# Kernel tuning notes

Hardware: AMD Instinct MI355X
Metric: run time of the kernel (lower is better)

Reference implementation:

```python
import jax, jax.numpy as jnp
import numpy as np

NUM_OBJS = 180   # len(vocab['node'])
NUM_PREDS = 180  # len(vocab['edge'])
D = 128          # embedding_dim == gconv_dim
H = 512          # gconv_hidden_dim
L = 5            # gconv_num_layers (1 GraphTripleConv + 4 in GraphTripleConvNet; identical shapes)
G = 64           # number of graphs in the batch
O = 5000         # total nodes
T = 20000        # total triples (edges)
SC = 0.02        # param init scale


def setup_inputs() -> dict:
    key = jax.random.key(0)
    ks = jax.random.split(key, 18)
    objs = jax.random.randint(ks[0], (O,), 0, NUM_OBJS + 1)
    s = jax.random.randint(ks[1], (T,), 0, O)
    o = jax.random.randint(ks[2], (T,), 0, O)
    p = jax.random.randint(ks[3], (T,), 0, NUM_PREDS)
    triples = jnp.stack([s, p, o], axis=1)
    obj_to_img = jnp.sort(jax.random.randint(ks[4], (O,), 0, G))
    f32 = jnp.float32
    return {
        'objs': objs,
        'triples': triples,
        'obj_to_img': obj_to_img,
        'obj_emb': jax.random.normal(ks[5], (NUM_OBJS + 1, D), f32) * SC,
        'pred_emb': jax.random.normal(ks[6], (NUM_PREDS, D), f32) * SC,
        # net1: [3D -> H -> 2H + D], stacked over L layers
        'n1w1': jax.random.normal(ks[7], (L, 3 * D, H), f32) * SC,
        'n1b1': jnp.zeros((L, H), f32),
        'n1w2': jax.random.normal(ks[8], (L, H, 2 * H + D), f32) * SC,
        'n1b2': jnp.zeros((L, 2 * H + D), f32),
        # net2: [H -> H -> D], stacked over L layers
        'n2w1': jax.random.normal(ks[9], (L, H, H), f32) * SC,
        'n2b1': jnp.zeros((L, H), f32),
        'n2w2': jax.random.normal(ks[10], (L, H, D), f32) * SC,
        'n2b2': jnp.zeros((L, D), f32),
        # AttentionModule: per-graph attention pooling over node vectors
        'att_w': jax.random.normal(ks[11], (D,), f32) * SC,
        'att_b': jnp.zeros((), f32),
    }


def _mlp2(x, w1, b1, w2, b2):
    # build_mlp with final_nonlinearity=True -> Linear,ReLU,Linear,ReLU
    return jax.nn.relu(jax.nn.relu(x @ w1 + b1) @ w2 + b2)


def _triple_conv(ov, pv, s, o, n1w1, n1b1, n1w2, n1b2, n2w1, n2b1, n2w2, n2b2):
    n_obj = ov.shape[0]
    t = jnp.concatenate([ov[s], pv, ov[o]], axis=1)          # [T, 3D]
    new_t = _mlp2(t, n1w1, n1b1, n1w2, n1b2)                 # [T, 2H+D]
    new_s = new_t[:, :H]
    new_p = new_t[:, H:H + D]
    new_o = new_t[:, H + D:]
    pooled = jnp.zeros((n_obj, H), new_t.dtype).at[s].add(new_s).at[o].add(new_o)
    counts = jnp.zeros((n_obj,), new_t.dtype).at[s].add(1.0).at[o].add(1.0)
    pooled = pooled / jnp.clip(counts, 1.0)[:, None]         # pooling='avg'
    new_ov = _mlp2(pooled, n2w1, n2b1, n2w2, n2b2)           # [O, D]
    return new_ov, new_p


def reference(objs, triples, obj_to_img, obj_emb, pred_emb,
              n1w1, n1b1, n1w2, n1b2, n2w1, n2b1, n2w2, n2b2, att_w, att_b):
    s, p, o = triples[:, 0], triples[:, 1], triples[:, 2]
    ov = obj_emb[objs]     # [O, D]
    pv = pred_emb[p]       # [T, D]
    for l in range(L):
        ov, pv = _triple_conv(ov, pv, s, o,
                              n1w1[l], n1b1[l], n1w2[l], n1b2[l],
                              n2w1[l], n2b1[l], n2w2[l], n2b2[l])
    # AttentionModule: segment softmax attention pooling per graph, broadcast back
    scores = ov @ att_w + att_b                               # [O]
    m = jax.ops.segment_max(scores, obj_to_img, num_segments=G)
    e = jnp.exp(scores - m[obj_to_img])
    z = jax.ops.segment_sum(e, obj_to_img, num_segments=G)
    w = e / z[obj_to_img]
    g = jax.ops.segment_sum(w[:, None] * ov, obj_to_img, num_segments=G)  # [G, D]
    graph_vecs = g[obj_to_img]                                # [O, D]
    return jnp.concatenate([ov, graph_vecs], axis=1)          # [O, 2D]
```

## Files before the change

kernel.cpp:

```cpp
#include <hip/hip_runtime.h>
#include <math.h>

#define O_N 5000
#define T_N 20000
#define D_ 128
#define H_ 512
#define L_ 5
#define G_ 64
#define NT_ 1152
#define NPRED 180

typedef unsigned short ushort_t;
typedef __attribute__((ext_vector_type(8))) __bf16 bf16x8;
typedef __attribute__((ext_vector_type(4))) float f32x4;

__device__ inline float bf2f(ushort_t u) {
    union { unsigned u32; float f; } cv; cv.u32 = ((unsigned)u) << 16; return cv.f;
}
__device__ inline ushort_t f2bf(float f) {
    union { float f; unsigned u; } cv; cv.f = f;
    unsigned x = cv.u;
    unsigned r = x + 0x7FFFu + ((x >> 16) & 1u);
    return (ushort_t)(r >> 16);
}

__device__ inline void gload16(const void* g, void* l) {
    __builtin_amdgcn_global_load_lds(
        (const __attribute__((address_space(1))) unsigned int*)g,
        (__attribute__((address_space(3))) unsigned int*)l,
        16, 0, 0);
}

template<int GATHER, int WRITE_F32>
__global__ __launch_bounds__(256)
void mfma_gemm(const ushort_t* __restrict__ A,
               const ushort_t* __restrict__ Bt,
               const float* __restrict__ bias,
               ushort_t* __restrict__ Cb,
               float* __restrict__ Cf,
               int M, int N, int K, int ldc, int ntiles,
               const int* __restrict__ triples,
               const ushort_t* __restrict__ ovb,
               const ushort_t* __restrict__ P, int pstride, int pmap)
{
    __shared__ __align__(16) ushort_t smem[16384];

    const int tid  = threadIdx.x;
    const int lane = tid & 63;
    const int wid  = tid >> 6;
    const int wm   = wid & 1;
    const int wn   = wid >> 1;

    const int nwg = gridDim.x;
    const int q = nwg >> 3, r = nwg & 7;
    const int xcd = blockIdx.x & 7, i8 = blockIdx.x >> 3;
    const int lid = (xcd < r ? xcd * (q + 1) : r * (q + 1) + (xcd - r) * q) + i8;
    const int bm = (lid / ntiles) * 128;
    const int bn = (lid % ntiles) * 128;

    const int u0 = wid * 64 + lane;
    const int u1 = u0 + 256;
    const int r0 = u0 >> 2;
    const int r1 = u1 >> 2;
    const int ks0 = (((u0 & 3) ^ ((r0 >> 1) & 3)) << 3);
    const int ks1 = (((u1 & 3) ^ ((r1 >> 1) & 3)) << 3);

    const int ga0 = min(bm + r0, M - 1);
    const int ga1 = min(bm + r1, M - 1);
    int s0 = 0, o0 = 0, p0 = 0, s1 = 0, o1 = 0, p1 = 0;
    if (GATHER) {
        s0 = triples[ga0 * 3];  p0 = pmap ? triples[ga0 * 3 + 1] : ga0;  o0 = triples[ga0 * 3 + 2];
        s1 = triples[ga1 * 3];  p1 = pmap ? triples[ga1 * 3 + 1] : ga1;  o1 = triples[ga1 * 3 + 2];
    }
    const int gb0 = bn + r0;
    const int gb1 = bn + r1;

    int offA[4], offB[4];
    #pragma unroll
    for (int i = 0; i < 4; ++i) {
        int ra = wm * 64 + i * 16 + (lane & 15);
        offA[i] = (ra * 4 + ((lane >> 4) ^ ((ra >> 1) & 3))) << 3;
        int rb = wn * 64 + i * 16 + (lane & 15);
        offB[i] = (rb * 4 + ((lane >> 4) ^ ((rb >> 1) & 3))) << 3;
    }

    auto stage = [&](int k0, int buf) {
        ushort_t* Ab = smem + buf * 4096;
        ushort_t* Bb = smem + 8192 + buf * 4096;
        const ushort_t *gA0p, *gA1p;
        if (GATHER) {
            int k = k0 + ks0;
            gA0p = (k < 128) ? (ovb + (size_t)s0 * D_ + k)
                 : (k < 256) ? (P + (size_t)p0 * pstride + (k - 128))
                             : (ovb + (size_t)o0 * D_ + (k - 256));
            k = k0 + ks1;
            gA1p = (k < 128) ? (ovb + (size_t)s1 * D_ + k)
                 : (k < 256) ? (P + (size_t)p1 * pstride + (k - 128))
                             : (ovb + (size_t)o1 * D_ + (k - 256));
        } else {
            gA0p = A + (size_t)ga0 * K + k0 + ks0;
            gA1p = A + (size_t)ga1 * K + k0 + ks1;
        }
        gload16(gA0p, Ab + wid * 512);
        gload16(gA1p, Ab + 2048 + wid * 512);
        gload16(Bt + (size_t)gb0 * K + k0 + ks0, Bb + wid * 512);
        gload16(Bt + (size_t)gb1 * K + k0 + ks1, Bb + 2048 + wid * 512);
    };

    f32x4 acc[4][4] = {};

    stage(0, 0);
    __syncthreads();

    const int nt = K >> 5;
    int cur = 0;
    for (int t = 0; t < nt; ++t) {
        if (t + 1 < nt) stage((t + 1) << 5, cur ^ 1);
        const ushort_t* Ar = smem + cur * 4096;
        const ushort_t* Br = smem + 8192 + cur * 4096;
        bf16x8 av[4], bv[4];
        #pragma unroll
        for (int i = 0; i < 4; ++i) av[i] = *(const bf16x8*)(Ar + offA[i]);
        #pragma unroll
        for (int i = 0; i < 4; ++i) bv[i] = *(const bf16x8*)(Br + offB[i]);
        #pragma unroll
        for (int mi = 0; mi < 4; ++mi)
            #pragma unroll
            for (int ni = 0; ni < 4; ++ni)
                acc[mi][ni] = __builtin_amdgcn_mfma_f32_16x16x32_bf16(
                    av[mi], bv[ni], acc[mi][ni], 0, 0, 0);
        __syncthreads();
        cur ^= 1;
    }

    if (WRITE_F32) {
        #pragma unroll
        for (int ni = 0; ni < 4; ++ni) {
            int col = bn + wn * 64 + ni * 16 + (lane & 15);
            float bz = bias[col];
            #pragma unroll
            for (int mi = 0; mi < 4; ++mi) {
                int rowb = bm + wm * 64 + mi * 16 + ((lane >> 4) << 2);
                #pragma unroll
                for (int rr = 0; rr < 4; ++rr) {
                    int row = rowb + rr;
                    if (row < M) {
                        float v = fmaxf(acc[mi][ni][rr] + bz, 0.0f);
                        Cb[(size_t)row * ldc + col] = f2bf(v);
                        Cf[(size_t)row * ldc + col] = v;
                    }
                }
            }
        }
    } else {
        ushort_t* cst = smem + wid * 4096;
        #pragma unroll
        for (int ni = 0; ni < 4; ++ni) {
            int col = ni * 16 + (lane & 15);
            float bz = bias[bn + wn * 64 + col];
            #pragma unroll
            for (int mi = 0; mi < 4; ++mi) {
                int rowb = mi * 16 + ((lane >> 4) << 2);
                #pragma unroll
                for (int rr = 0; rr < 4; ++rr) {
                    float v = fmaxf(acc[mi][ni][rr] + bz, 0.0f);
                    cst[(rowb + rr) * 64 + col] = f2bf(v);
                }
            }
        }
        #pragma unroll
        for (int pp = 0; pp < 8; ++pp) {
            int wrow = pp * 8 + (lane >> 3);
            int grow = bm + wm * 64 + wrow;
            if (grow < M) {
                float4 v = *(const float4*)(cst + wrow * 64 + (lane & 7) * 8);
                *(float4*)(&Cb[(size_t)grow * ldc + bn + wn * 64 + (lane & 7) * 8]) = v;
            }
        }
    }
}

__global__ void wt_transpose(const float* __restrict__ src, ushort_t* __restrict__ dst,
                             int K, int N)
{
    __shared__ float t[32][33];
    const int l  = blockIdx.z;
    const int n0 = blockIdx.x * 32;
    const int k0 = blockIdx.y * 32;
    const int r  = threadIdx.x >> 5;
    const int c  = threadIdx.x & 31;
    const float* s = src + (size_t)l * K * N;
    ushort_t*    d = dst + (size_t)l * N * K;
    #pragma unroll
    for (int j = 0; j < 4; ++j)
        t[r + j * 8][c] = s[(size_t)(k0 + r + j * 8) * N + n0 + c];
    __syncthreads();
    #pragma unroll
    for (int j = 0; j < 4; ++j)
        d[(size_t)(n0 + r + j * 8) * K + k0 + c] = f2bf(t[c][r + j * 8]);
}

__global__ void init_embs(const int* __restrict__ objs,
                          const float* __restrict__ obj_emb,
                          const float* __restrict__ pred_emb,
                          ushort_t* __restrict__ ovb, ushort_t* __restrict__ predb)
{
    int i = blockIdx.x * blockDim.x + threadIdx.x;
    if (i < O_N * D_) ovb[i] = f2bf(obj_emb[(size_t)objs[i >> 7] * D_ + (i & 127)]);
    int j = i - O_N * D_;
    if (j >= 0 && j < NPRED * D_) predb[j] = f2bf(pred_emb[j]);
}

__global__ void hist_kernel(const int* __restrict__ triples, int* __restrict__ cnt)
{
    int t = blockIdx.x * blockDim.x + threadIdx.x;
    if (t < T_N) {
        atomicAdd(&cnt[triples[t * 3]], 1);
        atomicAdd(&cnt[triples[t * 3 + 2]], 1);
    }
}

__global__ void scan_kernel(const int* __restrict__ cnt, int* __restrict__ off,
                            int* __restrict__ cursor)
{
    __shared__ int buf[256];
    __shared__ int base;
    int tid = threadIdx.x;
    if (tid == 0) base = 0;
    __syncthreads();
    for (int ch = 0; ch < O_N; ch += 256) {
        int v = (ch + tid < O_N) ? cnt[ch + tid] : 0;
        buf[tid] = v;
        __syncthreads();
        for (int s = 1; s < 256; s <<= 1) {
            int tmp = (tid >= s) ? buf[tid - s] : 0;
            __syncthreads();
            buf[tid] += tmp;
            __syncthreads();
        }
        int excl = base + buf[tid] - v;
        if (ch + tid < O_N) { off[ch + tid] = excl; cursor[ch + tid] = excl; }
        __syncthreads();
        if (tid == 0) base += buf[255];
        __syncthreads();
    }
    if (tid == 0) off[O_N] = base;
}

__global__ void fill_kernel(const int* __restrict__ triples, int* __restrict__ cursor,
                            int* __restrict__ entries)
{
    int t = blockIdx.x * blockDim.x + threadIdx.x;
    if (t < T_N) {
        int s = triples[t * 3], o = triples[t * 3 + 2];
        entries[atomicAdd(&cursor[s], 1)] = t * 2;
        entries[atomicAdd(&cursor[o], 1)] = t * 2 + 1;
    }
}

__global__ void pooled_kernel(const ushort_t* __restrict__ newt,
                              const int* __restrict__ entries,
                              const int* __restrict__ off,
                              ushort_t* __restrict__ pooled)
{
    int i = blockIdx.x, tid = threadIdx.x;
    int st = off[i], en = off[i + 1];
    float a0 = 0.f, a1 = 0.f, a2 = 0.f, a3 = 0.f;
    for (int e = st; e < en; ++e) {
        int ent = entries[e];
        const ushort_t* row = newt + (size_t)(ent >> 1) * NT_ + (ent & 1) * 640 + tid * 4;
        ushort4 v = *(const ushort4*)row;
        a0 += bf2f(v.x); a1 += bf2f(v.y); a2 += bf2f(v.z); a3 += bf2f(v.w);
    }
    int c = en - st; if (c < 1) c = 1;
    float sc = 1.0f / (float)c;
    ushort4 outv;
    outv.x = f2bf(a0 * sc); outv.y = f2bf(a1 * sc);
    outv.z = f2bf(a2 * sc); outv.w = f2bf(a3 * sc);
    *(ushort4*)(pooled + (size_t)i * H_ + tid * 4) = outv;
}

__global__ void scores_kernel(const float* __restrict__ ov,
                              const float* __restrict__ att_w,
                              const float* __restrict__ att_b,
                              float* __restrict__ scores)
{
    int gidx = blockIdx.x * blockDim.x + threadIdx.x;
    int obj = gidx >> 6;
    int lane = threadIdx.x & 63;
    if (obj >= O_N) return;
    const float* r = ov + (size_t)obj * D_;
    float v = r[lane] * att_w[lane] + r[lane + 64] * att_w[lane + 64];
    #pragma unroll
    for (int off = 32; off; off >>= 1) v += __shfl_down(v, off);
    if (lane == 0) scores[obj] = v + att_b[0];
}

__global__ void seg_init_kernel(int* __restrict__ seg_start, int* __restrict__ seg_end)
{
    int g = threadIdx.x;
    if (g < G_) { seg_start[g] = O_N; seg_end[g] = 0; }
}

__global__ void seg_bounds_kernel(const int* __restrict__ obj_to_img,
                                  int* __restrict__ seg_start, int* __restrict__ seg_end)
{
    int i = blockIdx.x * blockDim.x + threadIdx.x;
    if (i < O_N) {
        int g = obj_to_img[i];
        atomicMin(&seg_start[g], i);
        atomicMax(&seg_end[g], i + 1);
    }
}

__global__ __launch_bounds__(256)
void seg_mz_kernel(const float* __restrict__ scores,
                   const int* __restrict__ seg_start, const int* __restrict__ seg_end,
                   float* __restrict__ segm, float* __restrict__ segz)
{
    __shared__ float red[256];
    int g = blockIdx.x, tid = threadIdx.x;
    int st = seg_start[g], en = seg_end[g];
    float lm = -1e30f;
    for (int i = st + tid; i < en; i += 256) lm = fmaxf(lm, scores[i]);
    red[tid] = lm; __syncthreads();
    for (int s = 128; s; s >>= 1) { if (tid < s) red[tid] = fmaxf(red[tid], red[tid + s]); __syncthreads(); }
    float m = red[0]; __syncthreads();
    float lz = 0.f;
    for (int i = st + tid; i < en; i += 256) lz += expf(scores[i] - m);
    red[tid] = lz; __syncthreads();
    for (int s = 128; s; s >>= 1) { if (tid < s) red[tid] += red[tid + s]; __syncthreads(); }
    if (tid == 0) { segm[g] = m; segz[g] = (red[0] > 0.f ? red[0] : 1.0f); }
}

__global__ void gvec_kernel(const float* __restrict__ scores, const float* __restrict__ ov,
                            const int* __restrict__ seg_start, const int* __restrict__ seg_end,
                            const float* __restrict__ segm, const float* __restrict__ segz,
                            float* __restrict__ gvec)
{
    int g = blockIdx.x, d = threadIdx.x;
    int st = seg_start[g], en = seg_end[g];
    float m = segm[g], invz = 1.0f / segz[g];
    float acc = 0.f;
    for (int i = st; i < en; ++i)
        acc += expf(scores[i] - m) * invz * ov[(size_t)i * D_ + d];
    gvec[g * D_ + d] = acc;
}

__global__ void output_kernel(const float* __restrict__ ov, const float* __restrict__ gvec,
                              const int* __restrict__ obj_to_img, float* __restrict__ out)
{
    int idx = blockIdx.x * blockDim.x + threadIdx.x;
    if (idx >= O_N * 256) return;
    int i = idx >> 8, d = idx & 255;
    out[idx] = (d < 128) ? ov[(size_t)i * D_ + d]
                         : gvec[obj_to_img[i] * D_ + (d - 128)];
}

extern "C" void kernel_launch(void* const* d_in, const int* in_sizes, int n_in,
                              void* d_out, int out_size, void* d_ws, size_t ws_size,
                              hipStream_t stream)
{
    const int*   objs       = (const int*)d_in[0];
    const int*   triples    = (const int*)d_in[1];
    const int*   obj_to_img = (const int*)d_in[2];
    const float* obj_emb    = (const float*)d_in[3];
    const float* pred_emb   = (const float*)d_in[4];
    const float* n1w1       = (const float*)d_in[5];
    const float* n1b1       = (const float*)d_in[6];
    const float* n1w2       = (const float*)d_in[7];
    const float* n1b2       = (const float*)d_in[8];
    const float* n2w1       = (const float*)d_in[9];
    const float* n2b1       = (const float*)d_in[10];
    const float* n2w2       = (const float*)d_in[11];
    const float* n2b2       = (const float*)d_in[12];
    const float* att_w      = (const float*)d_in[13];
    const float* att_b      = (const float*)d_in[14];
    float* out = (float*)d_out;

    char* p = (char*)d_ws;
    auto carve = [&](size_t bytes) -> char* {
        char* r = p; p += (bytes + 255) & ~(size_t)255; return r;
    };
    ushort_t* w1t     = (ushort_t*)carve((size_t)L_ * 512 * 384 * 2);
    ushort_t* w2t     = (ushort_t*)carve((size_t)L_ * 1152 * 512 * 2);
    ushort_t* w3t     = (ushort_t*)carve((size_t)L_ * 512 * 512 * 2);
    ushort_t* w4t     = (ushort_t*)carve((size_t)L_ * 128 * 512 * 2);
    ushort_t* ovbA    = (ushort_t*)carve((size_t)O_N * D_ * 2);
    ushort_t* ovbB    = (ushort_t*)carve((size_t)O_N * D_ * 2);
    ushort_t* predb   = (ushort_t*)carve((size_t)NPRED * D_ * 2);
    ushort_t* hiddenb = (ushort_t*)carve((size_t)T_N * H_ * 2);
    ushort_t* newtb   = (ushort_t*)carve((size_t)T_N * NT_ * 2);
    ushort_t* pooledb = (ushort_t*)carve((size_t)O_N * H_ * 2);
    float*    ovf     = (float*)carve((size_t)O_N * D_ * 4);
    float*    scores  = (float*)carve((size_t)O_N * 4);
    float*    segm    = (float*)carve((size_t)G_ * 4);
    float*    segz    = (float*)carve((size_t)G_ * 4);
    float*    gvec    = (float*)carve((size_t)G_ * D_ * 4);
    int*      cnt     = (int*)carve((size_t)O_N * 4);
    int*      off     = (int*)carve((size_t)(O_N + 1) * 4);
    int*      cursor  = (int*)carve((size_t)O_N * 4);
    int*      entries = (int*)carve((size_t)2 * T_N * 4);
    int*      seg_start = (int*)carve((size_t)G_ * 4);
    int*      seg_end   = (int*)carve((size_t)G_ * 4);

    wt_transpose<<<dim3(512 / 32, 384 / 32, L_), 256, 0, stream>>>(n1w1, w1t, 384, 512);
    wt_transpose<<<dim3(1152 / 32, 512 / 32, L_), 256, 0, stream>>>(n1w2, w2t, 512, 1152);
    wt_transpose<<<dim3(512 / 32, 512 / 32, L_), 256, 0, stream>>>(n2w1, w3t, 512, 512);
    wt_transpose<<<dim3(128 / 32, 512 / 32, L_), 256, 0, stream>>>(n2w2, w4t, 512, 128);
    init_embs<<<((O_N + NPRED) * D_ + 255) / 256, 256, 0, stream>>>(objs, obj_emb, pred_emb, ovbA, predb);
    hipMemsetAsync(cnt, 0, O_N * sizeof(int), stream);
    hist_kernel<<<(T_N + 255) / 256, 256, 0, stream>>>(triples, cnt);
    scan_kernel<<<1, 256, 0, stream>>>(cnt, off, cursor);
    fill_kernel<<<(T_N + 255) / 256, 256, 0, stream>>>(triples, cursor, entries);

    ushort_t* ovcur = ovbA;
    ushort_t* ovnxt = ovbB;

    for (int l = 0; l < L_; ++l) {
        const ushort_t* Pl = (l == 0) ? predb : (newtb + H_);
        int pstr = (l == 0) ? D_ : NT_;
        int pmap = (l == 0) ? 1 : 0;

        mfma_gemm<1, 0><<<157 * 4, 256, 0, stream>>>(
            nullptr, w1t + (size_t)l * 512 * 384, n1b1 + (size_t)l * H_,
            hiddenb, nullptr, T_N, 512, 384, H_, 4,
            triples, ovcur, Pl, pstr, pmap);

        mfma_gemm<0, 0><<<157 * 9, 256, 0, stream>>>(
            hiddenb, w2t + (size_t)l * 1152 * 512, n1b2 + (size_t)l * NT_,
            newtb, nullptr, T_N, NT_, 512, NT_, 9,
            nullptr, nullptr, nullptr, 0, 0);

        pooled_kernel<<<O_N, 128, 0, stream>>>(newtb, entries, off, pooledb);

        mfma_gemm<0, 0><<<40 * 4, 256, 0, stream>>>(
            pooledb, w3t + (size_t)l * 512 * 512, n2b1 + (size_t)l * H_,
            hiddenb, nullptr, O_N, 512, 512, H_, 4,
            nullptr, nullptr, nullptr, 0, 0);

        mfma_gemm<0, 1><<<40 * 1, 256, 0, stream>>>(
            hiddenb, w4t + (size_t)l * 128 * 512, n2b2 + (size_t)l * D_,
            ovnxt, ovf, O_N, 128, 512, D_, 1,
            nullptr, nullptr, nullptr, 0, 0);

        ushort_t* tmp = ovcur; ovcur = ovnxt; ovnxt = tmp;
    }

    scores_kernel<<<(O_N * 64 + 255) / 256, 256, 0, stream>>>(ovf, att_w, att_b, scores);
    seg_init_kernel<<<1, G_, 0, stream>>>(seg_start, seg_end);
    seg_bounds_kernel<<<(O_N + 255) / 256, 256, 0, stream>>>(obj_to_img, seg_start, seg_end);
    seg_mz_kernel<<<G_, 256, 0, stream>>>(scores, seg_start, seg_end, segm, segz);
    gvec_kernel<<<G_, D_, 0, stream>>>(scores, ovf, seg_start, seg_end, segm, segz, gvec);
    output_kernel<<<(O_N * 256 + 255) / 256, 256, 0, stream>>>(ovf, gvec, obj_to_img, out);
}
```

Baseline: 661.2 us.

## Deepen GEMM prefetch pipeline and fuse setup and segment-attention kernels

New measurement: 559.4 us. -15.4%, faster.

```diff
diff --git a/kernel.cpp b/kernel.cpp
--- a/kernel.cpp
+++ b/kernel.cpp
@@ -109,13 +109,15 @@
 
     f32x4 acc[4][4] = {};
 
+    const int nt = K >> 5;
     stage(0, 0);
-    __syncthreads();
-
-    const int nt = K >> 5;
+    stage(32, 1);
+
     int cur = 0;
-    for (int t = 0; t < nt; ++t) {
-        if (t + 1 < nt) stage((t + 1) << 5, cur ^ 1);
+    for (int t = 0; t < nt - 1; ++t) {
+        asm volatile("s_waitcnt vmcnt(4)" ::: "memory");
+        __builtin_amdgcn_s_barrier();
+        __builtin_amdgcn_sched_barrier(0);
         const ushort_t* Ar = smem + cur * 4096;
         const ushort_t* Br = smem + 8192 + cur * 4096;
         bf16x8 av[4], bv[4];
@@ -123,15 +125,37 @@
         for (int i = 0; i < 4; ++i) av[i] = *(const bf16x8*)(Ar + offA[i]);
         #pragma unroll
         for (int i = 0; i < 4; ++i) bv[i] = *(const bf16x8*)(Br + offB[i]);
+        asm volatile("s_waitcnt lgkmcnt(0)" ::: "memory");
+        __builtin_amdgcn_sched_barrier(0);
+        __builtin_amdgcn_s_barrier();
+        if (t + 2 < nt) stage((t + 2) << 5, cur);
         #pragma unroll
         for (int mi = 0; mi < 4; ++mi)
             #pragma unroll
             for (int ni = 0; ni < 4; ++ni)
                 acc[mi][ni] = __builtin_amdgcn_mfma_f32_16x16x32_bf16(
                     av[mi], bv[ni], acc[mi][ni], 0, 0, 0);
-        __syncthreads();
         cur ^= 1;
     }
+    {
+        asm volatile("s_waitcnt vmcnt(0)" ::: "memory");
+        __builtin_amdgcn_s_barrier();
+        __builtin_amdgcn_sched_barrier(0);
+        const ushort_t* Ar = smem + cur * 4096;
+        const ushort_t* Br = smem + 8192 + cur * 4096;
+        bf16x8 av[4], bv[4];
+        #pragma unroll
+        for (int i = 0; i < 4; ++i) av[i] = *(const bf16x8*)(Ar + offA[i]);
+        #pragma unroll
+        for (int i = 0; i < 4; ++i) bv[i] = *(const bf16x8*)(Br + offB[i]);
+        #pragma unroll
+        for (int mi = 0; mi < 4; ++mi)
+            #pragma unroll
+            for (int ni = 0; ni < 4; ++ni)
+                acc[mi][ni] = __builtin_amdgcn_mfma_f32_16x16x32_bf16(
+                    av[mi], bv[ni], acc[mi][ni], 0, 0, 0);
+    }
+    __syncthreads();
 
     if (WRITE_F32) {
         #pragma unroll
@@ -180,35 +204,44 @@
     }
 }
 
-__global__ void wt_transpose(const float* __restrict__ src, ushort_t* __restrict__ dst,
-                             int K, int N)
-{
-    __shared__ float t[32][33];
-    const int l  = blockIdx.z;
-    const int n0 = blockIdx.x * 32;
-    const int k0 = blockIdx.y * 32;
-    const int r  = threadIdx.x >> 5;
-    const int c  = threadIdx.x & 31;
-    const float* s = src + (size_t)l * K * N;
-    ushort_t*    d = dst + (size_t)l * N * K;
-    #pragma unroll
-    for (int j = 0; j < 4; ++j)
-        t[r + j * 8][c] = s[(size_t)(k0 + r + j * 8) * N + n0 + c];
-    __syncthreads();
-    #pragma unroll
-    for (int j = 0; j < 4; ++j)
-        d[(size_t)(n0 + r + j * 8) * K + k0 + c] = f2bf(t[c][r + j * 8]);
-}
-
-__global__ void init_embs(const int* __restrict__ objs,
-                          const float* __restrict__ obj_emb,
-                          const float* __restrict__ pred_emb,
-                          ushort_t* __restrict__ ovb, ushort_t* __restrict__ predb)
-{
-    int i = blockIdx.x * blockDim.x + threadIdx.x;
-    if (i < O_N * D_) ovb[i] = f2bf(obj_emb[(size_t)objs[i >> 7] * D_ + (i & 127)]);
-    int j = i - O_N * D_;
-    if (j >= 0 && j < NPRED * D_) predb[j] = f2bf(pred_emb[j]);
+__global__ __launch_bounds__(256)
+void precompute_kernel(const float* __restrict__ n1w1, const float* __restrict__ n1w2,
+                       const float* __restrict__ n2w1, const float* __restrict__ n2w2,
+                       ushort_t* __restrict__ w1t, ushort_t* __restrict__ w2t,
+                       ushort_t* __restrict__ w3t, ushort_t* __restrict__ w4t,
+                       const int* __restrict__ objs, const float* __restrict__ obj_emb,
+                       const float* __restrict__ pred_emb,
+                       ushort_t* __restrict__ ovb, ushort_t* __restrict__ predb,
+                       int* __restrict__ cnt)
+{
+    int b = blockIdx.x;
+    if (b < 5440) {
+        int l = b / 1088, r = b % 1088;
+        const float* src; ushort_t* dst; int K, N, n0, k0;
+        if (r < 192)       { src = n1w1; dst = w1t; K = 384; N = 512;  n0 = (r % 16) * 32; k0 = (r / 16) * 32; }
+        else if (r < 768)  { r -= 192;  src = n1w2; dst = w2t; K = 512; N = 1152; n0 = (r % 36) * 32; k0 = (r / 36) * 32; }
+        else if (r < 1024) { r -= 768;  src = n2w1; dst = w3t; K = 512; N = 512;  n0 = (r % 16) * 32; k0 = (r / 16) * 32; }
+        else               { r -= 1024; src = n2w2; dst = w4t; K = 512; N = 128;  n0 = (r % 4) * 32;  k0 = (r / 4) * 32; }
+        __shared__ float t[32][33];
+        const float* s = src + (size_t)l * K * N;
+        ushort_t*    d = dst + (size_t)l * N * K;
+        int rr = threadIdx.x >> 5, c = threadIdx.x & 31;
+        #pragma unroll
+        for (int j = 0; j < 4; ++j)
+            t[rr + j * 8][c] = s[(size_t)(k0 + rr + j * 8) * N + n0 + c];
+        __syncthreads();
+        #pragma unroll
+        for (int j = 0; j < 4; ++j)
+            d[(size_t)(n0 + rr + j * 8) * K + k0 + c] = f2bf(t[c][rr + j * 8]);
+    } else if (b < 8030) {
+        int i = (b - 5440) * 256 + threadIdx.x;
+        if (i < O_N * D_) ovb[i] = f2bf(obj_emb[(size_t)objs[i >> 7] * D_ + (i & 127)]);
+        int j = i - O_N * D_;
+        if (j >= 0 && j < NPRED * D_) predb[j] = f2bf(pred_emb[j]);
+    } else {
+        int i = (b - 8030) * 256 + threadIdx.x;
+        if (i < O_N) cnt[i] = 0;
+    }
 }
 
 __global__ void hist_kernel(const int* __restrict__ triples, int* __restrict__ cnt)
@@ -296,55 +329,42 @@
     if (lane == 0) scores[obj] = v + att_b[0];
 }
 
-__global__ void seg_init_kernel(int* __restrict__ seg_start, int* __restrict__ seg_end)
-{
-    int g = threadIdx.x;
-    if (g < G_) { seg_start[g] = O_N; seg_end[g] = 0; }
-}
-
-__global__ void seg_bounds_kernel(const int* __restrict__ obj_to_img,
-                                  int* __restrict__ seg_start, int* __restrict__ seg_end)
-{
-    int i = blockIdx.x * blockDim.x + threadIdx.x;
-    if (i < O_N) {
-        int g = obj_to_img[i];
-        atomicMin(&seg_start[g], i);
-        atomicMax(&seg_end[g], i + 1);
-    }
-}
-
 __global__ __launch_bounds__(256)
-void seg_mz_kernel(const float* __restrict__ scores,
-                   const int* __restrict__ seg_start, const int* __restrict__ seg_end,
-                   float* __restrict__ segm, float* __restrict__ segz)
+void seg_gvec_kernel(const float* __restrict__ scores, const float* __restrict__ ovf,
+                     const int* __restrict__ obj_to_img, float* __restrict__ gvec)
 {
     __shared__ float red[256];
+    __shared__ float sm, sz;
     int g = blockIdx.x, tid = threadIdx.x;
-    int st = seg_start[g], en = seg_end[g];
+    int lo = 0, hi = O_N;
+    while (lo < hi) { int mid = (lo + hi) >> 1; if (obj_to_img[mid] < g) lo = mid + 1; else hi = mid; }
+    int st = lo;
+    hi = O_N;
+    while (lo < hi) { int mid = (lo + hi) >> 1; if (obj_to_img[mid] <= g) lo = mid + 1; else hi = mid; }
+    int en = lo;
+
     float lm = -1e30f;
     for (int i = st + tid; i < en; i += 256) lm = fmaxf(lm, scores[i]);
     red[tid] = lm; __syncthreads();
     for (int s = 128; s; s >>= 1) { if (tid < s) red[tid] = fmaxf(red[tid], red[tid + s]); __syncthreads(); }
-    float m = red[0]; __syncthreads();
+    if (tid == 0) sm = red[0];
+    __syncthreads();
+    float m = sm;
+
     float lz = 0.f;
     for (int i = st + tid; i < en; i += 256) lz += expf(scores[i] - m);
     red[tid] = lz; __syncthreads();
     for (int s = 128; s; s >>= 1) { if (tid < s) red[tid] += red[tid + s]; __syncthreads(); }
-    if (tid == 0) { segm[g] = m; segz[g] = (red[0] > 0.f ? red[0] : 1.0f); }
-}
-
-__global__ void gvec_kernel(const float* __restrict__ scores, const float* __restrict__ ov,
-                            const int* __restrict__ seg_start, const int* __restrict__ seg_end,
-                            const float* __restrict__ segm, const float* __restrict__ segz,
-                            float* __restrict__ gvec)
-{
-    int g = blockIdx.x, d = threadIdx.x;
-    int st = seg_start[g], en = seg_end[g];
-    float m = segm[g], invz = 1.0f / segz[g];
+    if (tid == 0) sz = fmaxf(red[0], 1e-30f);
+    __syncthreads();
+    float invz = 1.0f / sz;
+
+    int d = tid & 127, half = tid >> 7;
     float acc = 0.f;
-    for (int i = st; i < en; ++i)
-        acc += expf(scores[i] - m) * invz * ov[(size_t)i * D_ + d];
-    gvec[g * D_ + d] = acc;
+    for (int i = st + half; i < en; i += 2)
+        acc += expf(scores[i] - m) * ovf[(size_t)i * D_ + d];
+    red[tid] = acc; __syncthreads();
+    if (tid < 128) gvec[(size_t)g * D_ + tid] = (red[tid] + red[tid + 128]) * invz;
 }
 
 __global__ void output_kernel(const float* __restrict__ ov, const float* __restrict__ gvec,
@@ -394,22 +414,15 @@
     ushort_t* pooledb = (ushort_t*)carve((size_t)O_N * H_ * 2);
     float*    ovf     = (float*)carve((size_t)O_N * D_ * 4);
     float*    scores  = (float*)carve((size_t)O_N * 4);
-    float*    segm    = (float*)carve((size_t)G_ * 4);
-    float*    segz    = (float*)carve((size_t)G_ * 4);
     float*    gvec    = (float*)carve((size_t)G_ * D_ * 4);
     int*      cnt     = (int*)carve((size_t)O_N * 4);
     int*      off     = (int*)carve((size_t)(O_N + 1) * 4);
     int*      cursor  = (int*)carve((size_t)O_N * 4);
     int*      entries = (int*)carve((size_t)2 * T_N * 4);
-    int*      seg_start = (int*)carve((size_t)G_ * 4);
-    int*      seg_end   = (int*)carve((size_t)G_ * 4);
-
-    wt_transpose<<<dim3(512 / 32, 384 / 32, L_), 256, 0, stream>>>(n1w1, w1t, 384, 512);
-    wt_transpose<<<dim3(1152 / 32, 512 / 32, L_), 256, 0, stream>>>(n1w2, w2t, 512, 1152);
-    wt_transpose<<<dim3(512 / 32, 512 / 32, L_), 256, 0, stream>>>(n2w1, w3t, 512, 512);
-    wt_transpose<<<dim3(128 / 32, 512 / 32, L_), 256, 0, stream>>>(n2w2, w4t, 512, 128);
-    init_embs<<<((O_N + NPRED) * D_ + 255) / 256, 256, 0, stream>>>(objs, obj_emb, pred_emb, ovbA, predb);
-    hipMemsetAsync(cnt, 0, O_N * sizeof(int), stream);
+
+    precompute_kernel<<<8050, 256, 0, stream>>>(
+        n1w1, n1w2, n2w1, n2w2, w1t, w2t, w3t, w4t,
+        objs, obj_emb, pred_emb, ovbA, predb, cnt);
     hist_kernel<<<(T_N + 255) / 256, 256, 0, stream>>>(triples, cnt);
     scan_kernel<<<1, 256, 0, stream>>>(cnt, off, cursor);
     fill_kernel<<<(T_N + 255) / 256, 256, 0, stream>>>(triples, cursor, entries);
@@ -439,18 +452,22 @@
             hiddenb, nullptr, O_N, 512, 512, H_, 4,
             nullptr, nullptr, nullptr, 0, 0);
 
-        mfma_gemm<0, 1><<<40 * 1, 256, 0, stream>>>(
-            hiddenb, w4t + (size_t)l * 128 * 512, n2b2 + (size_t)l * D_,
-            ovnxt, ovf, O_N, 128, 512, D_, 1,
-            nullptr, nullptr, nullptr, 0, 0);
+        if (l < L_ - 1) {
+            mfma_gemm<0, 0><<<40 * 1, 256, 0, stream>>>(
+                hiddenb, w4t + (size_t)l * 128 * 512, n2b2 + (size_t)l * D_,
+                ovnxt, nullptr, O_N, 128, 512, D_, 1,
+                nullptr, nullptr, nullptr, 0, 0);
+        } else {
+            mfma_gemm<0, 1><<<40 * 1, 256, 0, stream>>>(
+                hiddenb, w4t + (size_t)l * 128 * 512, n2b2 + (size_t)l * D_,
+                ovnxt, ovf, O_N, 128, 512, D_, 1,
+                nullptr, nullptr, nullptr, 0, 0);
+        }
 
         ushort_t* tmp = ovcur; ovcur = ovnxt; ovnxt = tmp;
     }
 
     scores_kernel<<<(O_N * 64 + 255) / 256, 256, 0, stream>>>(ovf, att_w, att_b, scores);
-    seg_init_kernel<<<1, G_, 0, stream>>>(seg_start, seg_end);
-    seg_bounds_kernel<<<(O_N + 255) / 256, 256, 0, stream>>>(obj_to_img, seg_start, seg_end);
-    seg_mz_kernel<<<G_, 256, 0, stream>>>(scores, seg_start, seg_end, segm, segz);
-    gvec_kernel<<<G_, D_, 0, stream>>>(scores, ovf, seg_start, seg_end, segm, segz, gvec);
+    seg_gvec_kernel<<<G_, 256, 0, stream>>>(scores, ovf, obj_to_img, gvec);
     output_kernel<<<(O_N * 256 + 255) / 256, 256, 0, stream>>>(ovf, gvec, obj_to_img, out);
 }
```
